# Optimization experiments

Hardware: AMD Instinct MI355X
Metric: run time of the kernel (lower is better)

The kernel has to match this reference:

```python
import jax, jax.numpy as jnp
import numpy as np

H = 8
HD = 64
RHO = 0.1


def setup_inputs() -> dict:
    key = jax.random.key(0)
    ks = jax.random.split(key, 5)
    B, L, D = 4, 512, 512
    x = jax.random.normal(ks[0], (B, L, D), dtype=jnp.float32)
    # store projection weights as [in, out] so y = x @ W (equivalent to torch Linear with W.T)
    Wq = jax.random.normal(ks[1], (D, H * HD), dtype=jnp.float32) * 0.02
    Wk = jax.random.normal(ks[2], (D, H * HD), dtype=jnp.float32) * 0.02
    Wv = jax.random.normal(ks[3], (D, H * HD), dtype=jnp.float32) * 0.02
    Wo = jax.random.normal(ks[4], (H * HD, D), dtype=jnp.float32) * 0.02
    return {"x": x, "Wq": Wq, "Wk": Wk, "Wv": Wv, "Wo": Wo}


def _build_adjacency(S):
    # S: [B, H, L, L]. A = (1/L) sum_j [thresholded outer(S[:,:,:,j]) / HD with zero diag]
    B, Hn, L, _ = S.shape
    eye = jnp.eye(L, dtype=bool)
    S_cols = jnp.transpose(S, (3, 0, 1, 2))  # [L, B, H, L]

    def step(acc, s_col):
        # s_col: [B, H, L]; U_j[i,k] = s_col[i] * s_col[k] / HD
        U = s_col[..., :, None] * s_col[..., None, :] / HD  # [B,H,L,L]
        U = jnp.where(eye, 0.0, U)
        A_j = jnp.where(U > RHO, U, 0.0)
        return acc + A_j, None

    A_sum, _ = jax.lax.scan(step, jnp.zeros_like(S), S_cols)
    return A_sum / L


def _normalize_adjacency(A):
    L = A.shape[-1]
    A_tilde = A + jnp.eye(L, dtype=A.dtype)
    D = jnp.clip(A_tilde.sum(axis=-1, keepdims=True), 1e-6, None)
    D_inv_sqrt = D ** -0.5  # [B,H,L,1]
    return D_inv_sqrt * A_tilde * jnp.swapaxes(D_inv_sqrt, -1, -2)


def reference(x, Wq, Wk, Wv, Wo):
    B, L, D = x.shape
    scale = jnp.sqrt(jnp.asarray(HD, dtype=x.dtype))
    def proj(W):
        return jnp.einsum('bld,de->ble', x, W).reshape(B, L, H, HD).transpose(0, 2, 1, 3)
    Q, K, V = proj(Wq), proj(Wk), proj(Wv)  # [B,H,L,HD]
    S = jnp.einsum('bhid,bhjd->bhij', Q, K)  # [B,H,L,L]
    A = _build_adjacency(S)
    A_hat = _normalize_adjacency(A)
    # jump: Phi(S) = A_hat @ S @ A_hat^T
    S_jump = jnp.einsum('bhij,bhjk,bhlk->bhil', A_hat, S, A_hat) / scale
    attn = jax.nn.softmax(S_jump, axis=-1)
    out = jnp.einsum('bhij,bhjd->bhid', attn, V)  # [B,H,L,HD]
    out = out.transpose(0, 2, 1, 3).reshape(B, L, H * HD)
    return jnp.einsum('ble,ed->bld', out, Wo)
```

## Files before the change

kernel.cpp:

```cpp
#include <hip/hip_runtime.h>
#include <math.h>


typedef __attribute__((ext_vector_type(8))) short short8v;
typedef __attribute__((ext_vector_type(4))) float f32x4;

__device__ __forceinline__ void split8(const float* v, unsigned* hi, unsigned* lo)
{
    #pragma unroll
    for (int q = 0; q < 4; ++q) {
        const unsigned b0 = __float_as_uint(v[2 * q])     & 0xFFFF0000u;
        const unsigned b1 = __float_as_uint(v[2 * q + 1]) & 0xFFFF0000u;
        const float d0 = v[2 * q]     - __uint_as_float(b0);
        const float d1 = v[2 * q + 1] - __uint_as_float(b1);
        hi[q] = (b0 >> 16) | b1;
        lo[q] = (__float_as_uint(d0) >> 16) | (__float_as_uint(d1) & 0xFFFF0000u);
    }
}

template<int BT>
__global__ __launch_bounds__(256)
void gemm_mfma(const float* __restrict__ Ap, const float* __restrict__ Bp,
               float* __restrict__ Cp, int K, int lda, int ldb, int ldc,
               long sA, long sB, long sC, float scale)
{
    const float* __restrict__ A = Ap + (long)blockIdx.z * sA;
    const float* __restrict__ B = Bp + (long)blockIdx.z * sB;
    float* __restrict__ C = Cp + (long)blockIdx.z * sC;
    const int m0 = blockIdx.y << 7, n0 = blockIdx.x << 7;

    __shared__ short Ah[128 * 32], Al[128 * 32], Bh[128 * 32], Bl[128 * 32];

    const int tid = threadIdx.x;
    const int lane = tid & 63, wv = tid >> 6;
    const int wr = wv >> 1, wc = wv & 1;

    f32x4 acc[4][4] = {};

    for (int k0 = 0; k0 < K; k0 += 32) {
        {
            const int row = tid >> 1;
            const int swz = (row & 3) ^ ((row >> 2) & 3);
            #pragma unroll
            for (int gg = 0; gg < 2; ++gg) {
                const int g = ((tid & 1) << 1) + gg;
                const float* src = A + (long)(m0 + row) * lda + k0 + (g << 3);
                float v[8];
                *(float4*)&v[0] = *(const float4*)src;
                *(float4*)&v[4] = *(const float4*)(src + 4);
                unsigned hi[4], lo[4];
                split8(v, hi, lo);
                const int off = row * 32 + ((g ^ swz) << 3);
                *(uint4*)&Ah[off] = *(uint4*)hi;
                *(uint4*)&Al[off] = *(uint4*)lo;
            }
        }
        if (BT) {
            const int row = tid >> 1;
            const int swz = (row & 3) ^ ((row >> 2) & 3);
            #pragma unroll
            for (int gg = 0; gg < 2; ++gg) {
                const int g = ((tid & 1) << 1) + gg;
                const float* src = B + (long)(n0 + row) * ldb + k0 + (g << 3);
                float v[8];
                *(float4*)&v[0] = *(const float4*)src;
                *(float4*)&v[4] = *(const float4*)(src + 4);
                unsigned hi[4], lo[4];
                split8(v, hi, lo);
                const int off = row * 32 + ((g ^ swz) << 3);
                *(uint4*)&Bh[off] = *(uint4*)hi;
                *(uint4*)&Bl[off] = *(uint4*)lo;
            }
        } else {
            const int n = tid & 127;
            const int swz = (n & 3) ^ ((n >> 2) & 3);
            #pragma unroll
            for (int gg = 0; gg < 2; ++gg) {
                const int g = ((tid >> 7) << 1) + gg;
                float v[8];
                #pragma unroll
                for (int e = 0; e < 8; ++e)
                    v[e] = B[(long)(k0 + (g << 3) + e) * ldb + n0 + n];
                unsigned hi[4], lo[4];
                split8(v, hi, lo);
                const int off = n * 32 + ((g ^ swz) << 3);
                *(uint4*)&Bh[off] = *(uint4*)hi;
                *(uint4*)&Bl[off] = *(uint4*)lo;
            }
        }
        __syncthreads();

        {
            const int r = lane & 15, g = lane >> 4;
            const int lswz = (r & 3) ^ ((r >> 2) & 3);
            const int gslot = ((g ^ lswz) << 3);
            const int abase = ((wr << 6) + r) * 32 + gslot;
            const int bbase = ((wc << 6) + r) * 32 + gslot;
            short8v afh[4], afl[4], bfh[4], bfl[4];
            #pragma unroll
            for (int f = 0; f < 4; ++f) {
                afh[f] = *(short8v*)&Ah[abase + f * 512];
                afl[f] = *(short8v*)&Al[abase + f * 512];
                bfh[f] = *(short8v*)&Bh[bbase + f * 512];
                bfl[f] = *(short8v*)&Bl[bbase + f * 512];
            }
            #pragma unroll
            for (int fi = 0; fi < 4; ++fi)
                #pragma unroll
                for (int fj = 0; fj < 4; ++fj) {
                    acc[fi][fj] = __builtin_amdgcn_mfma_f32_16x16x32_bf16(
                        afh[fi], bfh[fj], acc[fi][fj], 0, 0, 0);
                    acc[fi][fj] = __builtin_amdgcn_mfma_f32_16x16x32_bf16(
                        afh[fi], bfl[fj], acc[fi][fj], 0, 0, 0);
                    acc[fi][fj] = __builtin_amdgcn_mfma_f32_16x16x32_bf16(
                        afl[fi], bfh[fj], acc[fi][fj], 0, 0, 0);
                }
        }
        __syncthreads();
    }

    const int r = lane & 15, g = lane >> 4;
    #pragma unroll
    for (int fi = 0; fi < 4; ++fi) {
        const int gr0 = m0 + (wr << 6) + fi * 16 + g * 4;
        #pragma unroll
        for (int fj = 0; fj < 4; ++fj) {
            const int gc = n0 + (wc << 6) + fj * 16 + r;
            #pragma unroll
            for (int qq = 0; qq < 4; ++qq)
                C[(long)(gr0 + qq) * ldc + gc] = acc[fi][fj][qq] * scale;
        }
    }
}

__global__ __launch_bounds__(256)
void gemm_qkv_mfma(const float* __restrict__ x, const float* __restrict__ Wq,
                   const float* __restrict__ Wk, const float* __restrict__ Wv,
                   float* __restrict__ QKV)
{
    const int m0 = blockIdx.y << 7;
    const int ng = blockIdx.x << 7;
    const float* __restrict__ W = (ng < 512) ? Wq : (ng < 1024) ? Wk : Wv;
    const int n0 = ng & 511;
    float* __restrict__ C = QKV + (long)(ng >> 9) * (1 << 20);

    __shared__ short Ah[128 * 32], Al[128 * 32], Bh[128 * 32], Bl[128 * 32];

    const int tid = threadIdx.x;
    const int lane = tid & 63, wv = tid >> 6;
    const int wr = wv >> 1, wc = wv & 1;

    f32x4 acc[4][4] = {};

    for (int k0 = 0; k0 < 512; k0 += 32) {
        {
            const int row = tid >> 1;
            const int swz = (row & 3) ^ ((row >> 2) & 3);
            #pragma unroll
            for (int gg = 0; gg < 2; ++gg) {
                const int g = ((tid & 1) << 1) + gg;
                const float* src = x + (long)(m0 + row) * 512 + k0 + (g << 3);
                float v[8];
                *(float4*)&v[0] = *(const float4*)src;
                *(float4*)&v[4] = *(const float4*)(src + 4);
                unsigned hi[4], lo[4];
                split8(v, hi, lo);
                const int off = row * 32 + ((g ^ swz) << 3);
                *(uint4*)&Ah[off] = *(uint4*)hi;
                *(uint4*)&Al[off] = *(uint4*)lo;
            }
        }
        {
            const int n = tid & 127;
            const int swz = (n & 3) ^ ((n >> 2) & 3);
            #pragma unroll
            for (int gg = 0; gg < 2; ++gg) {
                const int g = ((tid >> 7) << 1) + gg;
                float v[8];
                #pragma unroll
                for (int e = 0; e < 8; ++e)
                    v[e] = W[(long)(k0 + (g << 3) + e) * 512 + n0 + n];
                unsigned hi[4], lo[4];
                split8(v, hi, lo);
                const int off = n * 32 + ((g ^ swz) << 3);
                *(uint4*)&Bh[off] = *(uint4*)hi;
                *(uint4*)&Bl[off] = *(uint4*)lo;
            }
        }
        __syncthreads();

        {
            const int r = lane & 15, g = lane >> 4;
            const int lswz = (r & 3) ^ ((r >> 2) & 3);
            const int gslot = ((g ^ lswz) << 3);
            const int abase = ((wr << 6) + r) * 32 + gslot;
            const int bbase = ((wc << 6) + r) * 32 + gslot;
            short8v afh[4], afl[4], bfh[4], bfl[4];
            #pragma unroll
            for (int f = 0; f < 4; ++f) {
                afh[f] = *(short8v*)&Ah[abase + f * 512];
                afl[f] = *(short8v*)&Al[abase + f * 512];
                bfh[f] = *(short8v*)&Bh[bbase + f * 512];
                bfl[f] = *(short8v*)&Bl[bbase + f * 512];
            }
            #pragma unroll
            for (int fi = 0; fi < 4; ++fi)
                #pragma unroll
                for (int fj = 0; fj < 4; ++fj) {
                    acc[fi][fj] = __builtin_amdgcn_mfma_f32_16x16x32_bf16(
                        afh[fi], bfh[fj], acc[fi][fj], 0, 0, 0);
                    acc[fi][fj] = __builtin_amdgcn_mfma_f32_16x16x32_bf16(
                        afh[fi], bfl[fj], acc[fi][fj], 0, 0, 0);
                    acc[fi][fj] = __builtin_amdgcn_mfma_f32_16x16x32_bf16(
                        afl[fi], bfh[fj], acc[fi][fj], 0, 0, 0);
                }
        }
        __syncthreads();
    }

    const int r = lane & 15, g = lane >> 4;
    #pragma unroll
    for (int fi = 0; fi < 4; ++fi) {
        const int gr0 = m0 + (wr << 6) + fi * 16 + g * 4;
        #pragma unroll
        for (int fj = 0; fj < 4; ++fj) {
            const int nl = n0 + (wc << 6) + fj * 16 + r;
            const int h = nl >> 6, d = nl & 63;
            #pragma unroll
            for (int qq = 0; qq < 4; ++qq) {
                const int m = gr0 + qq;
                const int b = m >> 9, l = m & 511;
                C[((long)((b * 8 + h) * 512 + l)) * 64 + d] = acc[fi][fj][qq];
            }
        }
    }
}

__global__ __launch_bounds__(256)
void adj_kernel(const float* __restrict__ S, float* __restrict__ A)
{
    const int bh = blockIdx.y;
    const float* __restrict__ Sh = S + (long)bh * 262144;
    float* __restrict__ Ah = A + (long)bh * 262144;

    int ti = 0, rem = blockIdx.x;
    while (rem >= 8 - ti) { rem -= 8 - ti; ++ti; }
    const int tk = ti + rem;
    const int i0 = ti << 6, k0 = tk << 6;

    __shared__ float smem[8704];

    const int tid  = threadIdx.x;
    const int lane = tid & 63;
    const int wv   = tid >> 6;
    const int ly8  = (lane >> 3) << 3;
    const int lx8  = (lane & 7) << 3;
    const int r4   = lane >> 2;
    const int q    = lane & 3;

    float (*stgL)[68] = (float(*)[68])&smem[wv * 2176];
    float (*stgR)[68] = (float(*)[68])&smem[wv * 2176 + 1088];

    const float RHO64 = 0.1f * 64.0f;

    float acc[8][8] = {};
    const int jw = wv << 7;

    float4 la[4], ra[4], lb[4], rb[4];

    #pragma unroll
    for (int p = 0; p < 4; ++p) {
        la[p] = *(const float4*)(Sh + (long)(i0 + r4 + (p << 4)) * 512 + jw + (q << 2));
        ra[p] = *(const float4*)(Sh + (long)(k0 + r4 + (p << 4)) * 512 + jw + (q << 2));
    }

    for (int cc = 0; cc < 4; ++cc) {
        {
            const int j1 = jw + ((2 * cc + 1) << 4);
            #pragma unroll
            for (int p = 0; p < 4; ++p) {
                lb[p] = *(const float4*)(Sh + (long)(i0 + r4 + (p << 4)) * 512 + j1 + (q << 2));
                rb[p] = *(const float4*)(Sh + (long)(k0 + r4 + (p << 4)) * 512 + j1 + (q << 2));
            }
            #pragma unroll
            for (int p = 0; p < 4; ++p) {
                const int row = r4 + (p << 4);
                stgL[(q << 2) + 0][row] = la[p].x;
                stgL[(q << 2) + 1][row] = la[p].y;
                stgL[(q << 2) + 2][row] = la[p].z;
                stgL[(q << 2) + 3][row] = la[p].w;
                stgR[(q << 2) + 0][row] = ra[p].x;
                stgR[(q << 2) + 1][row] = ra[p].y;
                stgR[(q << 2) + 2][row] = ra[p].z;
                stgR[(q << 2) + 3][row] = ra[p].w;
            }
            asm volatile("s_waitcnt lgkmcnt(0)" ::: "memory");
            __builtin_amdgcn_sched_barrier(0);
            #pragma unroll 4
            for (int jj = 0; jj < 16; ++jj) {
                float a[8], b[8];
                *(float4*)&a[0] = *(const float4*)&stgL[jj][ly8];
                *(float4*)&a[4] = *(const float4*)&stgL[jj][ly8 + 4];
                *(float4*)&b[0] = *(const float4*)&stgR[jj][lx8];
                *(float4*)&b[4] = *(const float4*)&stgR[jj][lx8 + 4];
                #pragma unroll
                for (int i = 0; i < 8; ++i)
                    #pragma unroll
                    for (int j = 0; j < 8; ++j) {
                        const float u = a[i] * b[j];
                        if (u > RHO64) acc[i][j] += u;
                    }
            }
        }
        {
            if (cc < 3) {
                const int j2 = jw + ((2 * cc + 2) << 4);
                #pragma unroll
                for (int p = 0; p < 4; ++p) {
                    la[p] = *(const float4*)(Sh + (long)(i0 + r4 + (p << 4)) * 512 + j2 + (q << 2));
                    ra[p] = *(const float4*)(Sh + (long)(k0 + r4 + (p << 4)) * 512 + j2 + (q << 2));
                }
            }
            #pragma unroll
            for (int p = 0; p < 4; ++p) {
                const int row = r4 + (p << 4);
                stgL[(q << 2) + 0][row] = lb[p].x;
                stgL[(q << 2) + 1][row] = lb[p].y;
                stgL[(q << 2) + 2][row] = lb[p].z;
                stgL[(q << 2) + 3][row] = lb[p].w;
                stgR[(q << 2) + 0][row] = rb[p].x;
                stgR[(q << 2) + 1][row] = rb[p].y;
                stgR[(q << 2) + 2][row] = rb[p].z;
                stgR[(q << 2) + 3][row] = rb[p].w;
            }
            asm volatile("s_waitcnt lgkmcnt(0)" ::: "memory");
            __builtin_amdgcn_sched_barrier(0);
            #pragma unroll 4
            for (int jj = 0; jj < 16; ++jj) {
                float a[8], b[8];
                *(float4*)&a[0] = *(const float4*)&stgL[jj][ly8];
                *(float4*)&a[4] = *(const float4*)&stgL[jj][ly8 + 4];
                *(float4*)&b[0] = *(const float4*)&stgR[jj][lx8];
                *(float4*)&b[4] = *(const float4*)&stgR[jj][lx8 + 4];
                #pragma unroll
                for (int i = 0; i < 8; ++i)
                    #pragma unroll
                    for (int j = 0; j < 8; ++j) {
                        const float u = a[i] * b[j];
                        if (u > RHO64) acc[i][j] += u;
                    }
            }
        }
    }

    float* red0 = &smem[0];
    float* red1 = &smem[4352];

    __syncthreads();
    if (wv == 1 || wv == 2) {
        float* dst = (wv == 1 ? red0 : red1) + lane * 68;
        #pragma unroll
        for (int i = 0; i < 8; ++i) {
            *(float4*)(dst + i * 8)     = *(float4*)&acc[i][0];
            *(float4*)(dst + i * 8 + 4) = *(float4*)&acc[i][4];
        }
    }
    __syncthreads();
    if (wv == 0 || wv == 3) {
        const float* src = (wv == 0 ? red0 : red1) + lane * 68;
        #pragma unroll
        for (int i = 0; i < 8; ++i) {
            float4 p0 = *(const float4*)(src + i * 8);
            float4 p1 = *(const float4*)(src + i * 8 + 4);
            acc[i][0] += p0.x; acc[i][1] += p0.y; acc[i][2] += p0.z; acc[i][3] += p0.w;
            acc[i][4] += p1.x; acc[i][5] += p1.y; acc[i][6] += p1.z; acc[i][7] += p1.w;
        }
    }
    __syncthreads();
    if (wv == 3) {
        float* dst = red0 + lane * 68;
        #pragma unroll
        for (int i = 0; i < 8; ++i) {
            *(float4*)(dst + i * 8)     = *(float4*)&acc[i][0];
            *(float4*)(dst + i * 8 + 4) = *(float4*)&acc[i][4];
        }
    }
    __syncthreads();
    if (wv == 0) {
        const float* src = red0 + lane * 68;
        const float SC = 1.0f / 32768.0f;
        float f[8][8];
        #pragma unroll
        for (int i = 0; i < 8; ++i) {
            float4 p0 = *(const float4*)(src + i * 8);
            float4 p1 = *(const float4*)(src + i * 8 + 4);
            f[i][0] = (acc[i][0] + p0.x) * SC;
            f[i][1] = (acc[i][1] + p0.y) * SC;
            f[i][2] = (acc[i][2] + p0.z) * SC;
            f[i][3] = (acc[i][3] + p0.w) * SC;
            f[i][4] = (acc[i][4] + p1.x) * SC;
            f[i][5] = (acc[i][5] + p1.y) * SC;
            f[i][6] = (acc[i][6] + p1.z) * SC;
            f[i][7] = (acc[i][7] + p1.w) * SC;
        }
        if (ti == tk) {
            #pragma unroll
            for (int i = 0; i < 8; ++i)
                #pragma unroll
                for (int j = 0; j < 8; ++j)
                    if (ly8 + i == lx8 + j) f[i][j] = 0.0f;
        }
        #pragma unroll
        for (int i = 0; i < 8; ++i) {
            float* dst = Ah + (long)(i0 + ly8 + i) * 512 + k0 + lx8;
            *(float4*)dst       = make_float4(f[i][0], f[i][1], f[i][2], f[i][3]);
            *(float4*)(dst + 4) = make_float4(f[i][4], f[i][5], f[i][6], f[i][7]);
        }
        if (ti != tk) {
            #pragma unroll
            for (int j = 0; j < 8; ++j) {
                float* dst = Ah + (long)(k0 + lx8 + j) * 512 + i0 + ly8;
                *(float4*)dst       = make_float4(f[0][j], f[1][j], f[2][j], f[3][j]);
                *(float4*)(dst + 4) = make_float4(f[4][j], f[5][j], f[6][j], f[7][j]);
            }
        }
    }
}

__global__ __launch_bounds__(256)
void rowsum_kernel(const float* __restrict__ A, float* __restrict__ R)
{
    const int row = (blockIdx.x << 2) + (threadIdx.x >> 6);
    const int lane = threadIdx.x & 63;
    const float* p = A + (long)row * 512;
    float s = 0.0f;
    #pragma unroll
    for (int t = 0; t < 8; ++t) s += p[lane + (t << 6)];
    #pragma unroll
    for (int off = 32; off; off >>= 1) s += __shfl_xor(s, off, 64);
    if (lane == 0) R[row] = 1.0f / sqrtf(fmaxf(1.0f + s, 1e-6f));
}

__global__ __launch_bounds__(256)
void ahat_kernel(float* __restrict__ A, const float* __restrict__ R)
{
    const long i4 = ((long)blockIdx.x * 256 + threadIdx.x) << 2;
    const long off = i4 & 262143;
    const long bh = i4 >> 18;
    const int i = (int)(off >> 9);
    const int k = (int)(off & 511);
    const float ri = R[(bh << 9) + i];
    const float* Rk = R + (bh << 9) + k;
    float4 v = *(float4*)(A + i4);
    v.x = ri * Rk[0] * (v.x + ((k + 0) == i ? 1.0f : 0.0f));
    v.y = ri * Rk[1] * (v.y + ((k + 1) == i ? 1.0f : 0.0f));
    v.z = ri * Rk[2] * (v.z + ((k + 2) == i ? 1.0f : 0.0f));
    v.w = ri * Rk[3] * (v.w + ((k + 3) == i ? 1.0f : 0.0f));
    *(float4*)(A + i4) = v;
}

__global__ __launch_bounds__(256)
void softmax_kernel(float* __restrict__ P)
{
    const int row = (blockIdx.x << 2) + (threadIdx.x >> 6);
    const int lane = threadIdx.x & 63;
    float* p = P + (long)row * 512 + (lane << 3);
    float4 v0 = *(float4*)p;
    float4 v1 = *(float4*)(p + 4);
    float mx = fmaxf(fmaxf(fmaxf(v0.x, v0.y), fmaxf(v0.z, v0.w)),
                     fmaxf(fmaxf(v1.x, v1.y), fmaxf(v1.z, v1.w)));
    #pragma unroll
    for (int off = 32; off; off >>= 1) mx = fmaxf(mx, __shfl_xor(mx, off, 64));
    float e[8];
    e[0] = __expf(v0.x - mx); e[1] = __expf(v0.y - mx);
    e[2] = __expf(v0.z - mx); e[3] = __expf(v0.w - mx);
    e[4] = __expf(v1.x - mx); e[5] = __expf(v1.y - mx);
    e[6] = __expf(v1.z - mx); e[7] = __expf(v1.w - mx);
    float s = (((e[0] + e[1]) + (e[2] + e[3])) + ((e[4] + e[5]) + (e[6] + e[7])));
    #pragma unroll
    for (int off = 32; off; off >>= 1) s += __shfl_xor(s, off, 64);
    const float inv = 1.0f / s;
    *(float4*)p       = make_float4(e[0] * inv, e[1] * inv, e[2] * inv, e[3] * inv);
    *(float4*)(p + 4) = make_float4(e[4] * inv, e[5] * inv, e[6] * inv, e[7] * inv);
}

__global__ __launch_bounds__(256)
void gemm_pv_mfma(const float* __restrict__ P, const float* __restrict__ V,
                  float* __restrict__ Of)
{
    const int bh = blockIdx.z;
    const float* __restrict__ Pp = P + (long)bh * 262144;
    const float* __restrict__ Vp = V + (long)bh * 32768;
    const int bb = bh >> 3, hh = bh & 7;
    const int m0 = blockIdx.y << 7;

    __shared__ short Ph[128 * 32], Pl[128 * 32], Vh[64 * 32], Vl[64 * 32];

    const int tid = threadIdx.x;
    const int lane = tid & 63, wv = tid >> 6;

    f32x4 acc[2][4] = {};

    for (int k0 = 0; k0 < 512; k0 += 32) {
        {
            const int row = tid >> 1;
            const int swz = (row & 3) ^ ((row >> 2) & 3);
            #pragma unroll
            for (int gg = 0; gg < 2; ++gg) {
                const int g = ((tid & 1) << 1) + gg;
                const float* src = Pp + (long)(m0 + row) * 512 + k0 + (g << 3);
                float v[8];
                *(float4*)&v[0] = *(const float4*)src;
                *(float4*)&v[4] = *(const float4*)(src + 4);
                unsigned hi[4], lo[4];
                split8(v, hi, lo);
                const int off = row * 32 + ((g ^ swz) << 3);
                *(uint4*)&Ph[off] = *(uint4*)hi;
                *(uint4*)&Pl[off] = *(uint4*)lo;
            }
        }
        {
            const int n = tid & 63, g = tid >> 6;
            const int swz = (n & 3) ^ ((n >> 2) & 3);
            float v[8];
            #pragma unroll
            for (int e = 0; e < 8; ++e)
                v[e] = Vp[(long)(k0 + (g << 3) + e) * 64 + n];
            unsigned hi[4], lo[4];
            split8(v, hi, lo);
            const int off = n * 32 + ((g ^ swz) << 3);
            *(uint4*)&Vh[off] = *(uint4*)hi;
            *(uint4*)&Vl[off] = *(uint4*)lo;
        }
        __syncthreads();

        {
            const int r = lane & 15, g = lane >> 4;
            const int lswz = (r & 3) ^ ((r >> 2) & 3);
            const int gslot = ((g ^ lswz) << 3);
            short8v afh[2], afl[2], bfh[4], bfl[4];
            #pragma unroll
            for (int fi = 0; fi < 2; ++fi) {
                const int abase = ((wv << 5) + (fi << 4) + r) * 32 + gslot;
                afh[fi] = *(short8v*)&Ph[abase];
                afl[fi] = *(short8v*)&Pl[abase];
            }
            #pragma unroll
            for (int fj = 0; fj < 4; ++fj) {
                const int bbase = ((fj << 4) + r) * 32 + gslot;
                bfh[fj] = *(short8v*)&Vh[bbase];
                bfl[fj] = *(short8v*)&Vl[bbase];
            }
            #pragma unroll
            for (int fi = 0; fi < 2; ++fi)
                #pragma unroll
                for (int fj = 0; fj < 4; ++fj) {
                    acc[fi][fj] = __builtin_amdgcn_mfma_f32_16x16x32_bf16(
                        afh[fi], bfh[fj], acc[fi][fj], 0, 0, 0);
                    acc[fi][fj] = __builtin_amdgcn_mfma_f32_16x16x32_bf16(
                        afh[fi], bfl[fj], acc[fi][fj], 0, 0, 0);
                    acc[fi][fj] = __builtin_amdgcn_mfma_f32_16x16x32_bf16(
                        afl[fi], bfh[fj], acc[fi][fj], 0, 0, 0);
                }
        }
        __syncthreads();
    }

    const int r = lane & 15, g = lane >> 4;
    #pragma unroll
    for (int fi = 0; fi < 2; ++fi) {
        const int l0 = m0 + (wv << 5) + fi * 16 + g * 4;
        #pragma unroll
        for (int fj = 0; fj < 4; ++fj) {
            const int d = fj * 16 + r;
            #pragma unroll
            for (int qq = 0; qq < 4; ++qq)
                Of[((long)((bb << 9) + l0 + qq) << 9) + (hh << 6) + d] = acc[fi][fj][qq];
        }
    }
}

extern "C" void kernel_launch(void* const* d_in, const int* in_sizes, int n_in,
                              void* d_out, int out_size, void* d_ws, size_t ws_size,
                              hipStream_t stream)
{
    const float* x  = (const float*)d_in[0];
    const float* Wq = (const float*)d_in[1];
    const float* Wk = (const float*)d_in[2];
    const float* Wv = (const float*)d_in[3];
    const float* Wo = (const float*)d_in[4];
    float* out = (float*)d_out;

    float* ws = (float*)d_ws;
    float* Q  = ws;
    float* Kt = Q  + (1u << 20);
    float* V  = Kt + (1u << 20);
    float* S  = V  + (1u << 20);
    float* Am = S  + (8u << 20);
    float* T  = Am + (8u << 20);
    float* R  = T  + (8u << 20);

    dim3 blk(256);

    gemm_qkv_mfma<<<dim3(12, 16, 1), blk, 0, stream>>>(x, Wq, Wk, Wv, Q);

    gemm_mfma<1><<<dim3(4, 4, 32), blk, 0, stream>>>(Q, Kt, S, 64, 64, 64, 512,
                                                     32768, 32768, 262144, 1.0f);

    adj_kernel<<<dim3(36, 32), blk, 0, stream>>>(S, Am);

    rowsum_kernel<<<dim3(4096), blk, 0, stream>>>(Am, R);

    ahat_kernel<<<dim3(8192), blk, 0, stream>>>(Am, R);

    gemm_mfma<0><<<dim3(4, 4, 32), blk, 0, stream>>>(Am, S, T, 512, 512, 512, 512,
                                                     262144, 262144, 262144, 1.0f);

    gemm_mfma<1><<<dim3(4, 4, 32), blk, 0, stream>>>(T, Am, S, 512, 512, 512, 512,
                                                     262144, 262144, 262144, 0.125f);

    softmax_kernel<<<dim3(4096), blk, 0, stream>>>(S);

    gemm_pv_mfma<<<dim3(1, 4, 32), blk, 0, stream>>>(S, V, Q);

    gemm_mfma<0><<<dim3(4, 16, 1), blk, 0, stream>>>(Q, Wo, out, 512, 512, 512, 512,
                                                     0, 0, 0, 1.0f);
}
```

Before: 498.9 us.

## Share double-buffered S staging across waves in adjacency kernel to raise occupancy

```diff
diff --git a/kernel.cpp b/kernel.cpp
--- a/kernel.cpp
+++ b/kernel.cpp
@@ -236,7 +236,7 @@
     }
 }
 
-__global__ __launch_bounds__(256)
+__global__ __launch_bounds__(256, 4)
 void adj_kernel(const float* __restrict__ S, float* __restrict__ A)
 {
     const int bh = blockIdx.y;
@@ -248,61 +248,56 @@
     const int tk = ti + rem;
     const int i0 = ti << 6, k0 = tk << 6;
 
-    __shared__ float smem[8704];
+    __shared__ float smem[4352];
 
     const int tid  = threadIdx.x;
     const int lane = tid & 63;
     const int wv   = tid >> 6;
     const int ly8  = (lane >> 3) << 3;
     const int lx8  = (lane & 7) << 3;
-    const int r4   = lane >> 2;
-    const int q    = lane & 3;
-
-    float (*stgL)[68] = (float(*)[68])&smem[wv * 2176];
-    float (*stgR)[68] = (float(*)[68])&smem[wv * 2176 + 1088];
-
-    const float RHO64 = 0.1f * 64.0f;
+    const int row  = tid >> 2;
+    const int q    = tid & 3;
+
+    const float RHO64 = 6.4f;
 
     float acc[8][8] = {};
-    const int jw = wv << 7;
-
-    float4 la[4], ra[4], lb[4], rb[4];
-
-    #pragma unroll
-    for (int p = 0; p < 4; ++p) {
-        la[p] = *(const float4*)(Sh + (long)(i0 + r4 + (p << 4)) * 512 + jw + (q << 2));
-        ra[p] = *(const float4*)(Sh + (long)(k0 + r4 + (p << 4)) * 512 + jw + (q << 2));
-    }
-
-    for (int cc = 0; cc < 4; ++cc) {
-        {
-            const int j1 = jw + ((2 * cc + 1) << 4);
-            #pragma unroll
-            for (int p = 0; p < 4; ++p) {
-                lb[p] = *(const float4*)(Sh + (long)(i0 + r4 + (p << 4)) * 512 + j1 + (q << 2));
-                rb[p] = *(const float4*)(Sh + (long)(k0 + r4 + (p << 4)) * 512 + j1 + (q << 2));
-            }
-            #pragma unroll
-            for (int p = 0; p < 4; ++p) {
-                const int row = r4 + (p << 4);
-                stgL[(q << 2) + 0][row] = la[p].x;
-                stgL[(q << 2) + 1][row] = la[p].y;
-                stgL[(q << 2) + 2][row] = la[p].z;
-                stgL[(q << 2) + 3][row] = la[p].w;
-                stgR[(q << 2) + 0][row] = ra[p].x;
-                stgR[(q << 2) + 1][row] = ra[p].y;
-                stgR[(q << 2) + 2][row] = ra[p].z;
-                stgR[(q << 2) + 3][row] = ra[p].w;
-            }
-            asm volatile("s_waitcnt lgkmcnt(0)" ::: "memory");
-            __builtin_amdgcn_sched_barrier(0);
-            #pragma unroll 4
-            for (int jj = 0; jj < 16; ++jj) {
+
+    const float* srcL = Sh + (long)(i0 + row) * 512 + (q << 2);
+    const float* srcR = Sh + (long)(k0 + row) * 512 + (q << 2);
+
+    {
+        const float4 rl = *(const float4*)srcL;
+        const float4 rr = *(const float4*)srcR;
+        float* dL = &smem[0];
+        float* dR = &smem[1088];
+        dL[((q << 2) + 0) * 68 + row] = rl.x;
+        dL[((q << 2) + 1) * 68 + row] = rl.y;
+        dL[((q << 2) + 2) * 68 + row] = rl.z;
+        dL[((q << 2) + 3) * 68 + row] = rl.w;
+        dR[((q << 2) + 0) * 68 + row] = rr.x;
+        dR[((q << 2) + 1) * 68 + row] = rr.y;
+        dR[((q << 2) + 2) * 68 + row] = rr.z;
+        dR[((q << 2) + 3) * 68 + row] = rr.w;
+    }
+    __syncthreads();
+
+    for (int c = 0; c < 32; ++c) {
+        float4 rl, rr;
+        if (c < 31) {
+            rl = *(const float4*)(srcL + ((c + 1) << 4));
+            rr = *(const float4*)(srcR + ((c + 1) << 4));
+        }
+        {
+            const float* sL = &smem[(c & 1) * 2176];
+            const float* sR = &smem[(c & 1) * 2176 + 1088];
+            #pragma unroll
+            for (int jj = 0; jj < 4; ++jj) {
+                const int jrow = (wv << 2) + jj;
                 float a[8], b[8];
-                *(float4*)&a[0] = *(const float4*)&stgL[jj][ly8];
-                *(float4*)&a[4] = *(const float4*)&stgL[jj][ly8 + 4];
-                *(float4*)&b[0] = *(const float4*)&stgR[jj][lx8];
-                *(float4*)&b[4] = *(const float4*)&stgR[jj][lx8 + 4];
+                *(float4*)&a[0] = *(const float4*)&sL[jrow * 68 + ly8];
+                *(float4*)&a[4] = *(const float4*)&sL[jrow * 68 + ly8 + 4];
+                *(float4*)&b[0] = *(const float4*)&sR[jrow * 68 + lx8];
+                *(float4*)&b[4] = *(const float4*)&sR[jrow * 68 + lx8 + 4];
                 #pragma unroll
                 for (int i = 0; i < 8; ++i)
                     #pragma unroll
@@ -312,97 +307,67 @@
                     }
             }
         }
-        {
-            if (cc < 3) {
-                const int j2 = jw + ((2 * cc + 2) << 4);
-                #pragma unroll
-                for (int p = 0; p < 4; ++p) {
-                    la[p] = *(const float4*)(Sh + (long)(i0 + r4 + (p << 4)) * 512 + j2 + (q << 2));
-                    ra[p] = *(const float4*)(Sh + (long)(k0 + r4 + (p << 4)) * 512 + j2 + (q << 2));
-                }
-            }
-            #pragma unroll
-            for (int p = 0; p < 4; ++p) {
-                const int row = r4 + (p << 4);
-                stgL[(q << 2) + 0][row] = lb[p].x;
-                stgL[(q << 2) + 1][row] = lb[p].y;
-                stgL[(q << 2) + 2][row] = lb[p].z;
-                stgL[(q << 2) + 3][row] = lb[p].w;
-                stgR[(q << 2) + 0][row] = rb[p].x;
-                stgR[(q << 2) + 1][row] = rb[p].y;
-                stgR[(q << 2) + 2][row] = rb[p].z;
-                stgR[(q << 2) + 3][row] = rb[p].w;
-            }
-            asm volatile("s_waitcnt lgkmcnt(0)" ::: "memory");
-            __builtin_amdgcn_sched_barrier(0);
-            #pragma unroll 4
-            for (int jj = 0; jj < 16; ++jj) {
-                float a[8], b[8];
-                *(float4*)&a[0] = *(const float4*)&stgL[jj][ly8];
-                *(float4*)&a[4] = *(const float4*)&stgL[jj][ly8 + 4];
-                *(float4*)&b[0] = *(const float4*)&stgR[jj][lx8];
-                *(float4*)&b[4] = *(const float4*)&stgR[jj][lx8 + 4];
-                #pragma unroll
-                for (int i = 0; i < 8; ++i)
-                    #pragma unroll
-                    for (int j = 0; j < 8; ++j) {
-                        const float u = a[i] * b[j];
-                        if (u > RHO64) acc[i][j] += u;
-                    }
-            }
-        }
-    }
-
-    float* red0 = &smem[0];
-    float* red1 = &smem[4352];
-
-    __syncthreads();
-    if (wv == 1 || wv == 2) {
-        float* dst = (wv == 1 ? red0 : red1) + lane * 68;
-        #pragma unroll
-        for (int i = 0; i < 8; ++i) {
-            *(float4*)(dst + i * 8)     = *(float4*)&acc[i][0];
-            *(float4*)(dst + i * 8 + 4) = *(float4*)&acc[i][4];
-        }
-    }
-    __syncthreads();
-    if (wv == 0 || wv == 3) {
-        const float* src = (wv == 0 ? red0 : red1) + lane * 68;
-        #pragma unroll
-        for (int i = 0; i < 8; ++i) {
-            float4 p0 = *(const float4*)(src + i * 8);
-            float4 p1 = *(const float4*)(src + i * 8 + 4);
-            acc[i][0] += p0.x; acc[i][1] += p0.y; acc[i][2] += p0.z; acc[i][3] += p0.w;
-            acc[i][4] += p1.x; acc[i][5] += p1.y; acc[i][6] += p1.z; acc[i][7] += p1.w;
-        }
-    }
-    __syncthreads();
-    if (wv == 3) {
-        float* dst = red0 + lane * 68;
-        #pragma unroll
-        for (int i = 0; i < 8; ++i) {
-            *(float4*)(dst + i * 8)     = *(float4*)&acc[i][0];
-            *(float4*)(dst + i * 8 + 4) = *(float4*)&acc[i][4];
-        }
-    }
-    __syncthreads();
+        if (c < 31) {
+            float* dL = &smem[((c + 1) & 1) * 2176];
+            float* dR = &smem[((c + 1) & 1) * 2176 + 1088];
+            dL[((q << 2) + 0) * 68 + row] = rl.x;
+            dL[((q << 2) + 1) * 68 + row] = rl.y;
+            dL[((q << 2) + 2) * 68 + row] = rl.z;
+            dL[((q << 2) + 3) * 68 + row] = rl.w;
+            dR[((q << 2) + 0) * 68 + row] = rr.x;
+            dR[((q << 2) + 1) * 68 + row] = rr.y;
+            dR[((q << 2) + 2) * 68 + row] = rr.z;
+            dR[((q << 2) + 3) * 68 + row] = rr.w;
+        }
+        __syncthreads();
+    }
+
+    float* buf0 = &smem[0];
+    float* buf1 = &smem[1088];
+
+    #pragma unroll
+    for (int qp = 0; qp < 4; ++qp) {
+        __syncthreads();
+        if (wv == 1 || wv == 2) {
+            float* dst = (wv == 1 ? buf0 : buf1) + lane * 17;
+            #pragma unroll
+            for (int e = 0; e < 16; ++e)
+                dst[e] = acc[(qp << 1) + (e >> 3)][e & 7];
+        }
+        __syncthreads();
+        if (wv == 0 || wv == 3) {
+            const float* src = (wv == 0 ? buf0 : buf1) + lane * 17;
+            #pragma unroll
+            for (int e = 0; e < 16; ++e)
+                acc[(qp << 1) + (e >> 3)][e & 7] += src[e];
+        }
+    }
+    #pragma unroll
+    for (int qp = 0; qp < 4; ++qp) {
+        __syncthreads();
+        if (wv == 3) {
+            float* dst = buf0 + lane * 17;
+            #pragma unroll
+            for (int e = 0; e < 16; ++e)
+                dst[e] = acc[(qp << 1) + (e >> 3)][e & 7];
+        }
+        __syncthreads();
+        if (wv == 0) {
+            const float* src = buf0 + lane * 17;
+            #pragma unroll
+            for (int e = 0; e < 16; ++e)
+                acc[(qp << 1) + (e >> 3)][e & 7] += src[e];
+        }
+    }
+
     if (wv == 0) {
-        const float* src = red0 + lane * 68;
         const float SC = 1.0f / 32768.0f;
         float f[8][8];
         #pragma unroll
-        for (int i = 0; i < 8; ++i) {
-            float4 p0 = *(const float4*)(src + i * 8);
-            float4 p1 = *(const float4*)(src + i * 8 + 4);
-            f[i][0] = (acc[i][0] + p0.x) * SC;
-            f[i][1] = (acc[i][1] + p0.y) * SC;
-            f[i][2] = (acc[i][2] + p0.z) * SC;
-            f[i][3] = (acc[i][3] + p0.w) * SC;
-            f[i][4] = (acc[i][4] + p1.x) * SC;
-            f[i][5] = (acc[i][5] + p1.y) * SC;
-            f[i][6] = (acc[i][6] + p1.z) * SC;
-            f[i][7] = (acc[i][7] + p1.w) * SC;
-        }
+        for (int i = 0; i < 8; ++i)
+            #pragma unroll
+            for (int j = 0; j < 8; ++j)
+                f[i][j] = acc[i][j] * SC;
         if (ti == tk) {
             #pragma unroll
             for (int i = 0; i < 8; ++i)
```

New measurement: 662.9 us. 32.9% more time.

## Rewrite thresholded outer-product accumulation as clamped FMA plus packed counts

Applied to the files above, without the earlier changes.

```diff
diff --git a/kernel.cpp b/kernel.cpp
--- a/kernel.cpp
+++ b/kernel.cpp
@@ -261,97 +261,58 @@
     float (*stgL)[68] = (float(*)[68])&smem[wv * 2176];
     float (*stgR)[68] = (float(*)[68])&smem[wv * 2176 + 1088];
 
-    const float RHO64 = 0.1f * 64.0f;
-
-    float acc[8][8] = {};
+    const float nC = -6.4f;
+
+    float    T1[8][8] = {};
+    unsigned cnt[8][2] = {};
+
     const int jw = wv << 7;
-
-    float4 la[4], ra[4], lb[4], rb[4];
-
-    #pragma unroll
-    for (int p = 0; p < 4; ++p) {
-        la[p] = *(const float4*)(Sh + (long)(i0 + r4 + (p << 4)) * 512 + jw + (q << 2));
-        ra[p] = *(const float4*)(Sh + (long)(k0 + r4 + (p << 4)) * 512 + jw + (q << 2));
-    }
-
-    for (int cc = 0; cc < 4; ++cc) {
-        {
-            const int j1 = jw + ((2 * cc + 1) << 4);
-            #pragma unroll
-            for (int p = 0; p < 4; ++p) {
-                lb[p] = *(const float4*)(Sh + (long)(i0 + r4 + (p << 4)) * 512 + j1 + (q << 2));
-                rb[p] = *(const float4*)(Sh + (long)(k0 + r4 + (p << 4)) * 512 + j1 + (q << 2));
-            }
-            #pragma unroll
-            for (int p = 0; p < 4; ++p) {
-                const int row = r4 + (p << 4);
-                stgL[(q << 2) + 0][row] = la[p].x;
-                stgL[(q << 2) + 1][row] = la[p].y;
-                stgL[(q << 2) + 2][row] = la[p].z;
-                stgL[(q << 2) + 3][row] = la[p].w;
-                stgR[(q << 2) + 0][row] = ra[p].x;
-                stgR[(q << 2) + 1][row] = ra[p].y;
-                stgR[(q << 2) + 2][row] = ra[p].z;
-                stgR[(q << 2) + 3][row] = ra[p].w;
-            }
-            asm volatile("s_waitcnt lgkmcnt(0)" ::: "memory");
-            __builtin_amdgcn_sched_barrier(0);
-            #pragma unroll 4
-            for (int jj = 0; jj < 16; ++jj) {
-                float a[8], b[8];
-                *(float4*)&a[0] = *(const float4*)&stgL[jj][ly8];
-                *(float4*)&a[4] = *(const float4*)&stgL[jj][ly8 + 4];
-                *(float4*)&b[0] = *(const float4*)&stgR[jj][lx8];
-                *(float4*)&b[4] = *(const float4*)&stgR[jj][lx8 + 4];
-                #pragma unroll
-                for (int i = 0; i < 8; ++i)
-                    #pragma unroll
-                    for (int j = 0; j < 8; ++j) {
-                        const float u = a[i] * b[j];
-                        if (u > RHO64) acc[i][j] += u;
-                    }
-            }
-        }
-        {
-            if (cc < 3) {
-                const int j2 = jw + ((2 * cc + 2) << 4);
-                #pragma unroll
-                for (int p = 0; p < 4; ++p) {
-                    la[p] = *(const float4*)(Sh + (long)(i0 + r4 + (p << 4)) * 512 + j2 + (q << 2));
-                    ra[p] = *(const float4*)(Sh + (long)(k0 + r4 + (p << 4)) * 512 + j2 + (q << 2));
+    for (int c = 0; c < 8; ++c) {
+        const int j0 = jw + (c << 4);
+        float4 rl[4], rr[4];
+        #pragma unroll
+        for (int p = 0; p < 4; ++p) {
+            rl[p] = *(const float4*)(Sh + (long)(i0 + r4 + (p << 4)) * 512 + j0 + (q << 2));
+            rr[p] = *(const float4*)(Sh + (long)(k0 + r4 + (p << 4)) * 512 + j0 + (q << 2));
+        }
+        #pragma unroll
+        for (int p = 0; p < 4; ++p) {
+            const int row = r4 + (p << 4);
+            stgL[(q << 2) + 0][row] = rl[p].x;
+            stgL[(q << 2) + 1][row] = rl[p].y;
+            stgL[(q << 2) + 2][row] = rl[p].z;
+            stgL[(q << 2) + 3][row] = rl[p].w;
+            stgR[(q << 2) + 0][row] = rr[p].x;
+            stgR[(q << 2) + 1][row] = rr[p].y;
+            stgR[(q << 2) + 2][row] = rr[p].z;
+            stgR[(q << 2) + 3][row] = rr[p].w;
+        }
+        __builtin_amdgcn_s_waitcnt(0);
+        #pragma unroll 4
+        for (int jj = 0; jj < 16; ++jj) {
+            float a[8], b[8];
+            *(float4*)&a[0] = *(const float4*)&stgL[jj][ly8];
+            *(float4*)&a[4] = *(const float4*)&stgL[jj][ly8 + 4];
+            *(float4*)&b[0] = *(const float4*)&stgR[jj][lx8];
+            *(float4*)&b[4] = *(const float4*)&stgR[jj][lx8 + 4];
+            #pragma unroll
+            for (int i = 0; i < 8; ++i)
+                #pragma unroll
+                for (int j = 0; j < 8; ++j) {
+                    const float d = fmaf(a[i], b[j], nC);
+                    T1[i][j] += fmaxf(d, 0.0f);
+                    cnt[i][j >> 2] += (((unsigned)__float_as_int(d)) >> 31) << ((j & 3) << 3);
                 }
-            }
-            #pragma unroll
-            for (int p = 0; p < 4; ++p) {
-                const int row = r4 + (p << 4);
-                stgL[(q << 2) + 0][row] = lb[p].x;
-                stgL[(q << 2) + 1][row] = lb[p].y;
-                stgL[(q << 2) + 2][row] = lb[p].z;
-                stgL[(q << 2) + 3][row] = lb[p].w;
-                stgR[(q << 2) + 0][row] = rb[p].x;
-                stgR[(q << 2) + 1][row] = rb[p].y;
-                stgR[(q << 2) + 2][row] = rb[p].z;
-                stgR[(q << 2) + 3][row] = rb[p].w;
-            }
-            asm volatile("s_waitcnt lgkmcnt(0)" ::: "memory");
-            __builtin_amdgcn_sched_barrier(0);
-            #pragma unroll 4
-            for (int jj = 0; jj < 16; ++jj) {
-                float a[8], b[8];
-                *(float4*)&a[0] = *(const float4*)&stgL[jj][ly8];
-                *(float4*)&a[4] = *(const float4*)&stgL[jj][ly8 + 4];
-                *(float4*)&b[0] = *(const float4*)&stgR[jj][lx8];
-                *(float4*)&b[4] = *(const float4*)&stgR[jj][lx8 + 4];
-                #pragma unroll
-                for (int i = 0; i < 8; ++i)
-                    #pragma unroll
-                    for (int j = 0; j < 8; ++j) {
-                        const float u = a[i] * b[j];
-                        if (u > RHO64) acc[i][j] += u;
-                    }
-            }
-        }
-    }
+        }
+    }
+
+    #pragma unroll
+    for (int i = 0; i < 8; ++i)
+        #pragma unroll
+        for (int j = 0; j < 8; ++j) {
+            const unsigned neg = (cnt[i][j >> 2] >> ((j & 3) << 3)) & 255u;
+            T1[i][j] = fmaf(6.4f, (float)(128u - neg), T1[i][j]);
+        }
 
     float* red0 = &smem[0];
     float* red1 = &smem[4352];
@@ -361,8 +322,8 @@
         float* dst = (wv == 1 ? red0 : red1) + lane * 68;
         #pragma unroll
         for (int i = 0; i < 8; ++i) {
-            *(float4*)(dst + i * 8)     = *(float4*)&acc[i][0];
-            *(float4*)(dst + i * 8 + 4) = *(float4*)&acc[i][4];
+            *(float4*)(dst + i * 8)     = *(float4*)&T1[i][0];
+            *(float4*)(dst + i * 8 + 4) = *(float4*)&T1[i][4];
         }
     }
     __syncthreads();
@@ -372,8 +333,8 @@
         for (int i = 0; i < 8; ++i) {
             float4 p0 = *(const float4*)(src + i * 8);
             float4 p1 = *(const float4*)(src + i * 8 + 4);
-            acc[i][0] += p0.x; acc[i][1] += p0.y; acc[i][2] += p0.z; acc[i][3] += p0.w;
-            acc[i][4] += p1.x; acc[i][5] += p1.y; acc[i][6] += p1.z; acc[i][7] += p1.w;
+            T1[i][0] += p0.x; T1[i][1] += p0.y; T1[i][2] += p0.z; T1[i][3] += p0.w;
+            T1[i][4] += p1.x; T1[i][5] += p1.y; T1[i][6] += p1.z; T1[i][7] += p1.w;
         }
     }
     __syncthreads();
@@ -381,8 +342,8 @@
         float* dst = red0 + lane * 68;
         #pragma unroll
         for (int i = 0; i < 8; ++i) {
-            *(float4*)(dst + i * 8)     = *(float4*)&acc[i][0];
-            *(float4*)(dst + i * 8 + 4) = *(float4*)&acc[i][4];
+            *(float4*)(dst + i * 8)     = *(float4*)&T1[i][0];
+            *(float4*)(dst + i * 8 + 4) = *(float4*)&T1[i][4];
         }
     }
     __syncthreads();
@@ -394,14 +355,14 @@
         for (int i = 0; i < 8; ++i) {
             float4 p0 = *(const float4*)(src + i * 8);
             float4 p1 = *(const float4*)(src + i * 8 + 4);
-            f[i][0] = (acc[i][0] + p0.x) * SC;
-            f[i][1] = (acc[i][1] + p0.y) * SC;
-            f[i][2] = (acc[i][2] + p0.z) * SC;
-            f[i][3] = (acc[i][3] + p0.w) * SC;
-            f[i][4] = (acc[i][4] + p1.x) * SC;
-            f[i][5] = (acc[i][5] + p1.y) * SC;
-            f[i][6] = (acc[i][6] + p1.z) * SC;
-            f[i][7] = (acc[i][7] + p1.w) * SC;
+            f[i][0] = (T1[i][0] + p0.x) * SC;
+            f[i][1] = (T1[i][1] + p0.y) * SC;
+            f[i][2] = (T1[i][2] + p0.z) * SC;
+            f[i][3] = (T1[i][3] + p0.w) * SC;
+            f[i][4] = (T1[i][4] + p1.x) * SC;
+            f[i][5] = (T1[i][5] + p1.y) * SC;
+            f[i][6] = (T1[i][6] + p1.z) * SC;
+            f[i][7] = (T1[i][7] + p1.w) * SC;
         }
         if (ti == tk) {
             #pragma unroll
```

New measurement: 536.8 us. 1.08x slower.
